# Performance work log

Hardware: AMD Instinct MI355X
Metric: run time of the kernel (lower is better)

## Reference

```python
import jax, jax.numpy as jnp
import numpy as np

T, B, F = 4096, 6, 128
H1, H3 = 512, 128  # 32*16 and 16*8


def run_lstm(x, Wi, Wh, b, h0, c0):
    """Standard LSTM over time-major x: [T, B, Fin] -> seq [T, B, H], (h, c)."""
    def step(carry, xt):
        h, c = carry
        z = xt @ Wi + h @ Wh + b           # [B, 4H]
        i, f, g, o = jnp.split(z, 4, axis=-1)
        c = jax.nn.sigmoid(f) * c + jax.nn.sigmoid(i) * jnp.tanh(g)
        h = jax.nn.sigmoid(o) * jnp.tanh(c)
        return (h, c), h
    (h, c), seq = jax.lax.scan(step, (h0, c0), x)
    return seq, h, c


def setup_inputs() -> dict:
    key = jax.random.key(0)
    ks = jax.random.split(key, 12)
    s = lambda fan_in: 1.0 / np.sqrt(fan_in)
    inp = {
        "x":   jax.random.normal(ks[0], (T, B, F), jnp.float32),
        "Wi1": jax.random.uniform(ks[1], (F, 4 * H1), jnp.float32, -s(H1), s(H1)),
        "Wh1": jax.random.uniform(ks[2], (H1, 4 * H1), jnp.float32, -s(H1), s(H1)),
        "b1":  jax.random.uniform(ks[3], (4 * H1,), jnp.float32, -s(H1), s(H1)),
        "Wi2": jax.random.uniform(ks[4], (H1, 4 * H1), jnp.float32, -s(H1), s(H1)),
        "Wh2": jax.random.uniform(ks[5], (H1, 4 * H1), jnp.float32, -s(H1), s(H1)),
        "b2":  jax.random.uniform(ks[6], (4 * H1,), jnp.float32, -s(H1), s(H1)),
        "Wi3": jax.random.uniform(ks[7], (H1, 4 * H3), jnp.float32, -s(H3), s(H3)),
        "Wh3": jax.random.uniform(ks[8], (H3, 4 * H3), jnp.float32, -s(H3), s(H3)),
        "b3":  jax.random.uniform(ks[9], (4 * H3,), jnp.float32, -s(H3), s(H3)),
        "Wl":  jax.random.uniform(ks[10], (H3, 1), jnp.float32, -s(H3), s(H3)),
        "bl":  jax.random.uniform(ks[11], (1,), jnp.float32, -s(H3), s(H3)),
    }
    return inp


def reference(x, Wi1, Wh1, b1, Wi2, Wh2, b2, Wi3, Wh3, b3, Wl, bl):
    z1 = jnp.zeros((B, H1), x.dtype)
    z3 = jnp.zeros((B, H3), x.dtype)
    seq, h, c = run_lstm(x, Wi1, Wh1, b1, z1, z1)
    seq, h, c = run_lstm(seq, Wi2, Wh2, b2, h, c)   # lstm2 reuses lstm1 final state
    seq, h, c = run_lstm(seq, Wi3, Wh3, b3, z3, z3) # lstm3 starts fresh
    return seq[-1] @ Wl + bl                         # [B, 1]
```

## Files before the change

kernel.cpp:

```cpp
#include <hip/hip_runtime.h>

#define TT 4096
#define NB 6

typedef unsigned int uint;
typedef unsigned long long u64;

__device__ __forceinline__ u64 ldp(const u64* p) {
  return __hip_atomic_load(p, __ATOMIC_RELAXED, __HIP_MEMORY_SCOPE_AGENT);
}
__device__ __forceinline__ void stp(u64* p, float v, uint s) {
  u64 x = ((u64)s << 32) | (u64)__float_as_uint(v);
  __hip_atomic_store(p, x, __ATOMIC_RELAXED, __HIP_MEMORY_SCOPE_AGENT);
}
__device__ __forceinline__ uint ldf(const uint* p) {
  return __hip_atomic_load(p, __ATOMIC_RELAXED, __HIP_MEMORY_SCOPE_AGENT);
}
__device__ __forceinline__ void stf(uint* p, uint v) {
  __hip_atomic_store(p, v, __ATOMIC_RELAXED, __HIP_MEMORY_SCOPE_AGENT);
}

__device__ __forceinline__ float sigm(float x) { return 1.f / (1.f + __expf(-x)); }
__device__ __forceinline__ float ftanh(float x) {
  x = fminf(fmaxf(x, -15.f), 15.f);
  const float e = __expf(-2.f * x);
  return (1.f - e) / (1.f + e);
}

__device__ __forceinline__ void lds_wave_fence() {
  asm volatile("s_waitcnt lgkmcnt(0)" ::: "memory");
  __builtin_amdgcn_sched_barrier(0);
}

__device__ __forceinline__ void poll6(const u64* rs, uint st, float out[6]) {
  u64 a0;
  for (;;) {
    a0 = ldp(rs);
    if ((uint)(a0 >> 32) == st) break;
    __builtin_amdgcn_s_sleep(1);
  }
  u64 a1, a2, a3, a4, a5;
  for (;;) {
    a1 = ldp(rs + 1); a2 = ldp(rs + 2); a3 = ldp(rs + 3);
    a4 = ldp(rs + 4); a5 = ldp(rs + 5);
    if (((uint)(a1 >> 32) == st) & ((uint)(a2 >> 32) == st) &
        ((uint)(a3 >> 32) == st) & ((uint)(a4 >> 32) == st) &
        ((uint)(a5 >> 32) == st)) break;
    __builtin_amdgcn_s_sleep(1);
  }
  out[0] = __uint_as_float((uint)a0); out[1] = __uint_as_float((uint)a1);
  out[2] = __uint_as_float((uint)a2); out[3] = __uint_as_float((uint)a3);
  out[4] = __uint_as_float((uint)a4); out[5] = __uint_as_float((uint)a5);
}

__device__ __forceinline__ void fma6(const float* vp, float w, float acc[6]) {
  const float2 v0 = *(const float2*)(vp);
  const float2 v1 = *(const float2*)(vp + 2);
  const float2 v2 = *(const float2*)(vp + 4);
  acc[0] += v0.x * w; acc[1] += v0.y * w; acc[2] += v1.x * w;
  acc[3] += v1.y * w; acc[4] += v2.x * w; acc[5] += v2.y * w;
}

__global__ __launch_bounds__(512, 2) void k_l1(
    const float* __restrict__ x, const float* __restrict__ Wi,
    const float* __restrict__ Wh, const float* __restrict__ bias,
    u64* h1ring, u64* h2ring, float* c1fin, float* seq1) {
  __shared__ float xl[2][128 * 6];
  __shared__ float hl[512 * 6];
  __shared__ float zred[16 * 32 * 8];
  __shared__ float zfin[32 * 6];
  __shared__ float bs[32];
  const int tid = threadIdx.x, wg = blockIdx.x;
  const int lane = tid & 63, w = tid >> 6;
  const int half = lane >> 5, c = lane & 31;
  const int u0 = wg * 8;
  const int gcol = ((c >> 3) * 512) + u0 + (c & 7);
  float wh[32], wx[8];
  {
    const int kh = w * 64 + half * 32, kx = w * 16 + half * 8;
#pragma unroll
    for (int kk = 0; kk < 32; ++kk) wh[kk] = Wh[(size_t)(kh + kk) * 2048 + gcol];
#pragma unroll
    for (int kk = 0; kk < 8; ++kk) wx[kk] = Wi[(size_t)(kx + kk) * 2048 + gcol];
  }
  if (tid < 32) bs[tid] = bias[((tid >> 3) * 512) + u0 + (tid & 7)];
  const int gj = tid / 6, gb = tid % 6;
  float creg = 0.f;
  {
    const float v0 = x[tid];
    float v1 = 0.f;
    if (tid < 256) v1 = x[512 + tid];
    xl[0][(tid & 127) * 6 + (tid >> 7)] = v0;
    if (tid < 256) { const int i = 512 + tid; xl[0][(i & 127) * 6 + (i >> 7)] = v1; }
  }
  __syncthreads();

  for (int t = 0; t < TT; ++t) {
    const float* xn = x + (size_t)((t + 1 < TT) ? t + 1 : TT - 1) * 768;
    const float v0p = xn[tid];
    float v1p = 0.f;
    if (tid < 256) v1p = xn[512 + tid];
    float acc[6] = {0, 0, 0, 0, 0, 0};
    {
      const float* xb = xl[t & 1] + (size_t)(w * 16 + half * 8) * 6;
#pragma unroll
      for (int kk = 0; kk < 8; ++kk) fma6(xb + kk * 6, wx[kk], acc);
    }
    {
      float hv[6];
      poll6(h1ring + (size_t)((t + 7) & 7) * 3072 + tid * 6, (uint)t, hv);
      float* hp = hl + tid * 6;
      *(float2*)(hp) = make_float2(hv[0], hv[1]);
      *(float2*)(hp + 2) = make_float2(hv[2], hv[3]);
      *(float2*)(hp + 4) = make_float2(hv[4], hv[5]);
    }
    lds_wave_fence();
    {
      const float* hb = hl + (size_t)(w * 64 + half * 32) * 6;
#pragma unroll
      for (int kk = 0; kk < 32; ++kk) fma6(hb + kk * 6, wh[kk], acc);
    }
    {
      float* zr = zred + (size_t)((w * 2 + half) * 32 + c) * 8;
      *(float4*)zr = make_float4(acc[0], acc[1], acc[2], acc[3]);
      *(float2*)(zr + 4) = make_float2(acc[4], acc[5]);
    }
    {
      float* xs = xl[(t + 1) & 1];
      xs[(tid & 127) * 6 + (tid >> 7)] = v0p;
      if (tid < 256) { const int i = 512 + tid; xs[(i & 127) * 6 + (i >> 7)] = v1p; }
    }
    __syncthreads();
    if (tid < 192) {
      const int cc = tid / 6, bb = tid % 6;
      float s = 0.f;
#pragma unroll
      for (int p = 0; p < 16; ++p) s += zred[(p * 32 + cc) * 8 + bb];
      zfin[cc * 6 + bb] = s;
    }
    __syncthreads();
    if (tid < 48) {
      __builtin_amdgcn_s_setprio(1);
      const float zi = zfin[(0 * 8 + gj) * 6 + gb] + bs[0 * 8 + gj];
      const float zf = zfin[(1 * 8 + gj) * 6 + gb] + bs[1 * 8 + gj];
      const float zg = zfin[(2 * 8 + gj) * 6 + gb] + bs[2 * 8 + gj];
      const float zo = zfin[(3 * 8 + gj) * 6 + gb] + bs[3 * 8 + gj];
      creg = sigm(zf) * creg + sigm(zi) * ftanh(zg);
      const float hval = sigm(zo) * ftanh(creg);
      const int gu = u0 + gj;
      stp(h1ring + (size_t)(t & 7) * 3072 + gu * 6 + gb, hval, (uint)(t + 1));
      seq1[(size_t)t * 4096 + gu * 8 + gb] = hval;
      if (t == TT - 1) {
        stp(h2ring + (size_t)7 * 3072 + gu * 6 + gb, hval, 0u);
        c1fin[gu * 6 + gb] = creg;
      }
      __builtin_amdgcn_s_setprio(0);
    }
  }
}

__global__ __launch_bounds__(512, 2) void k_l23(
    const float* __restrict__ seq1, const float* __restrict__ Wi2,
    const float* __restrict__ Wh2, const float* __restrict__ b2,
    const float* __restrict__ Wi3, const float* __restrict__ Wh3,
    const float* __restrict__ b3, const float* __restrict__ c1fin,
    u64* h2ring, u64* h3ring, float* h3fin, uint* flags3) {
  __shared__ float smem[13536];
  const int tid = threadIdx.x, wg = blockIdx.x;
  const int lane = tid & 63, w = tid >> 6;
  const int gj = tid / 6, gb = tid % 6;

  if (wg < 64) {
    float* xls = smem;
    float* hl = smem + 6144;
    float* zred = smem + 9216;
    float* zfin = smem + 13312;
    float* bsl = smem + 13504;
    const int half = lane >> 5, c = lane & 31;
    const int u0 = wg * 8;
    const int gcol = ((c >> 3) * 512) + u0 + (c & 7);
    float wh[32], wx[32];
    {
      const int kb = w * 64 + half * 32;
#pragma unroll
      for (int kk = 0; kk < 32; ++kk) {
        wh[kk] = Wh2[(size_t)(kb + kk) * 2048 + gcol];
        wx[kk] = Wi2[(size_t)(kb + kk) * 2048 + gcol];
      }
    }
    if (tid < 32) bsl[tid] = b2[((tid >> 3) * 512) + u0 + (tid & 7)];
    float creg = (tid < 48) ? c1fin[(u0 + gj) * 6 + gb] : 0.f;
    {
      const float4 s0 = *(const float4*)(seq1 + (size_t)tid * 8);
      const float4 s1 = *(const float4*)(seq1 + (size_t)tid * 8 + 4);
      float* xs = xls;
      *(float2*)(xs + tid * 6) = make_float2(s0.x, s0.y);
      *(float2*)(xs + tid * 6 + 2) = make_float2(s0.z, s0.w);
      *(float2*)(xs + tid * 6 + 4) = make_float2(s1.x, s1.y);
    }
    __syncthreads();

    for (int t = 0; t < TT; ++t) {
      if ((t & 3) == 0 && t >= 8 && tid < 48) {
        const uint need = (uint)(t - 4);
        while (ldf(flags3 + (tid & 7)) < need) __builtin_amdgcn_s_sleep(1);
      }
      const float* sn = seq1 + (size_t)((t + 1 < TT) ? t + 1 : TT - 1) * 4096;
      const float4 p0 = *(const float4*)(sn + (size_t)tid * 8);
      const float4 p1 = *(const float4*)(sn + (size_t)tid * 8 + 4);
      float acc[6] = {0, 0, 0, 0, 0, 0};
      {
        const float* xb = xls + (size_t)(t & 1) * 3072 + (size_t)(w * 64 + half * 32) * 6;
#pragma unroll
        for (int kk = 0; kk < 32; ++kk) fma6(xb + kk * 6, wx[kk], acc);
      }
      {
        float hv[6];
        poll6(h2ring + (size_t)((t + 7) & 7) * 3072 + tid * 6, (uint)t, hv);
        float* hp = hl + tid * 6;
        *(float2*)(hp) = make_float2(hv[0], hv[1]);
        *(float2*)(hp + 2) = make_float2(hv[2], hv[3]);
        *(float2*)(hp + 4) = make_float2(hv[4], hv[5]);
      }
      lds_wave_fence();
      {
        const float* hb = hl + (size_t)(w * 64 + half * 32) * 6;
#pragma unroll
        for (int kk = 0; kk < 32; ++kk) fma6(hb + kk * 6, wh[kk], acc);
      }
      {
        float* zr = zred + (size_t)((w * 2 + half) * 32 + c) * 8;
        *(float4*)zr = make_float4(acc[0], acc[1], acc[2], acc[3]);
        *(float2*)(zr + 4) = make_float2(acc[4], acc[5]);
      }
      {
        float* xs = xls + (size_t)((t + 1) & 1) * 3072;
        *(float2*)(xs + tid * 6) = make_float2(p0.x, p0.y);
        *(float2*)(xs + tid * 6 + 2) = make_float2(p0.z, p0.w);
        *(float2*)(xs + tid * 6 + 4) = make_float2(p1.x, p1.y);
      }
      __syncthreads();
      if (tid < 192) {
        const int cc = tid / 6, bb = tid % 6;
        float s = 0.f;
#pragma unroll
        for (int p = 0; p < 16; ++p) s += zred[(p * 32 + cc) * 8 + bb];
        zfin[cc * 6 + bb] = s;
      }
      __syncthreads();
      if (tid < 48) {
        __builtin_amdgcn_s_setprio(1);
        const float zi = zfin[(0 * 8 + gj) * 6 + gb] + bsl[0 * 8 + gj];
        const float zf = zfin[(1 * 8 + gj) * 6 + gb] + bsl[1 * 8 + gj];
        const float zg = zfin[(2 * 8 + gj) * 6 + gb] + bsl[2 * 8 + gj];
        const float zo = zfin[(3 * 8 + gj) * 6 + gb] + bsl[3 * 8 + gj];
        creg = sigm(zf) * creg + sigm(zi) * ftanh(zg);
        const float hval = sigm(zo) * ftanh(creg);
        stp(h2ring + (size_t)(t & 7) * 3072 + (u0 + gj) * 6 + gb, hval, (uint)(t + 1));
        __builtin_amdgcn_s_setprio(0);
      }
    }
  } else {
    float* hl2 = smem;
    float* hl3 = smem + 3072;
    float* zred = smem + 3840;
    float* zfin = smem + 7936;
    float* bsl = smem + 8320;
    const int wg3 = wg - 64;
    const int c = lane;
    const int u0 = wg3 * 16;
    const int gcol = ((c >> 4) * 128) + u0 + (c & 15);
    float wxh2[64], wh3[16];
#pragma unroll
    for (int kk = 0; kk < 64; ++kk) wxh2[kk] = Wi3[(size_t)(w * 64 + kk) * 512 + gcol];
#pragma unroll
    for (int kk = 0; kk < 16; ++kk) wh3[kk] = Wh3[(size_t)(w * 16 + kk) * 512 + gcol];
    if (tid < 64) bsl[tid] = b3[((tid >> 4) * 128) + u0 + (tid & 15)];
    float creg = 0.f;

    for (int t = 0; t < TT; ++t) {
      {
        const u64* rs3 = h3ring + (size_t)((t + 7) & 7) * 768;
        const int a = 96 * w + lane;
        u64 v;
        for (;;) { v = ldp(rs3 + a); if ((uint)(v >> 32) == (uint)t) break; __builtin_amdgcn_s_sleep(1); }
        hl3[a] = __uint_as_float((uint)v);
        if (lane < 32) {
          const int a2 = a + 64;
          u64 v2;
          for (;;) { v2 = ldp(rs3 + a2); if ((uint)(v2 >> 32) == (uint)t) break; __builtin_amdgcn_s_sleep(1); }
          hl3[a2] = __uint_as_float((uint)v2);
        }
      }
      {
        float hv[6];
        poll6(h2ring + (size_t)(t & 7) * 3072 + tid * 6, (uint)(t + 1), hv);
        float* hp = hl2 + tid * 6;
        *(float2*)(hp) = make_float2(hv[0], hv[1]);
        *(float2*)(hp + 2) = make_float2(hv[2], hv[3]);
        *(float2*)(hp + 4) = make_float2(hv[4], hv[5]);
      }
      lds_wave_fence();
      float acc[6] = {0, 0, 0, 0, 0, 0};
      {
        const float* hb = hl2 + (size_t)(w * 64) * 6;
#pragma unroll
        for (int kk = 0; kk < 64; ++kk) fma6(hb + kk * 6, wxh2[kk], acc);
        const float* h3b = hl3 + (size_t)(w * 16) * 6;
#pragma unroll
        for (int kk = 0; kk < 16; ++kk) fma6(h3b + kk * 6, wh3[kk], acc);
      }
      {
        float* zr = zred + (size_t)(w * 64 + c) * 8;
        *(float4*)zr = make_float4(acc[0], acc[1], acc[2], acc[3]);
        *(float2*)(zr + 4) = make_float2(acc[4], acc[5]);
      }
      __syncthreads();
      if (tid == 0) stf(flags3 + wg3, (uint)(t + 1));
      if (tid < 384) {
        const int cc = tid / 6, bb = tid % 6;
        float s = 0.f;
#pragma unroll
        for (int p = 0; p < 8; ++p) s += zred[(p * 64 + cc) * 8 + bb];
        zfin[cc * 6 + bb] = s;
      }
      __syncthreads();
      if (tid < 96) {
        __builtin_amdgcn_s_setprio(1);
        const float zi = zfin[(0 * 16 + gj) * 6 + gb] + bsl[0 * 16 + gj];
        const float zf = zfin[(1 * 16 + gj) * 6 + gb] + bsl[1 * 16 + gj];
        const float zg = zfin[(2 * 16 + gj) * 6 + gb] + bsl[2 * 16 + gj];
        const float zo = zfin[(3 * 16 + gj) * 6 + gb] + bsl[3 * 16 + gj];
        creg = sigm(zf) * creg + sigm(zi) * ftanh(zg);
        const float hval = sigm(zo) * ftanh(creg);
        stp(h3ring + (size_t)(t & 7) * 768 + (u0 + gj) * 6 + gb, hval, (uint)(t + 1));
        if (t == TT - 1) h3fin[(u0 + gj) * 6 + gb] = hval;
        __builtin_amdgcn_s_setprio(0);
      }
    }
  }
}

__global__ void k_out(const float* __restrict__ h3fin, const float* __restrict__ Wl,
                      const float* __restrict__ bl, float* __restrict__ out) {
  const int tid = threadIdx.x;
  float p[NB] = {0, 0, 0, 0, 0, 0};
  for (int k = tid; k < 128; k += 64) {
    const float w = Wl[k];
#pragma unroll
    for (int b = 0; b < NB; ++b) p[b] += h3fin[k * 6 + b] * w;
  }
#pragma unroll
  for (int off = 32; off > 0; off >>= 1) {
#pragma unroll
    for (int b = 0; b < NB; ++b) p[b] += __shfl_down(p[b], off);
  }
  if (tid == 0) {
#pragma unroll
    for (int b = 0; b < NB; ++b) out[b] = p[b] + bl[0];
  }
}

extern "C" void kernel_launch(void* const* d_in, const int* in_sizes, int n_in,
                              void* d_out, int out_size, void* d_ws, size_t ws_size,
                              hipStream_t stream) {
  (void)in_sizes; (void)n_in; (void)out_size;
  const float* x   = (const float*)d_in[0];
  const float* Wi1 = (const float*)d_in[1];
  const float* Wh1 = (const float*)d_in[2];
  const float* b1  = (const float*)d_in[3];
  const float* Wi2 = (const float*)d_in[4];
  const float* Wh2 = (const float*)d_in[5];
  const float* b2  = (const float*)d_in[6];
  const float* Wi3 = (const float*)d_in[7];
  const float* Wh3 = (const float*)d_in[8];
  const float* b3  = (const float*)d_in[9];
  const float* Wl  = (const float*)d_in[10];
  const float* bl  = (const float*)d_in[11];

  char* wsb = (char*)d_ws;
  u64*  h1ring = (u64*)(wsb + 0);
  u64*  h2ring = (u64*)(wsb + 196608);
  u64*  h3ring = (u64*)(wsb + 393216);
  float* c1fin = (float*)(wsb + 442368);
  float* h3fin = (float*)(wsb + 454656);
  uint* flags3 = (uint*)(wsb + 457728);
  float* seq1  = (float*)(wsb + 458752);

  const size_t need = 458752 + (size_t)TT * 512 * 8 * sizeof(float);
  if (ws_size < need) {
    hipMemsetAsync(d_out, 0, 6 * sizeof(float), stream);
    return;
  }

  hipMemsetAsync(d_ws, 0, 458752, stream);

  k_l1<<<64, 512, 0, stream>>>(x, Wi1, Wh1, b1, h1ring, h2ring, c1fin, seq1);
  k_l23<<<72, 512, 0, stream>>>(seq1, Wi2, Wh2, b2, Wi3, Wh3, b3, c1fin,
                                h2ring, h3ring, h3fin, flags3);
  k_out<<<1, 64, 0, stream>>>(h3fin, Wl, bl, (float*)d_out);
}
```

Before: 44.91 ms.

## Halve workgroup count with 16 units per block and fuse gate reduction

Layer-1 and layer-2 blocks now each own 16 hidden units instead of 8. Each thread holds 64 recurrent weights in registers, and each wave covers a full K slice, so fewer blocks take part in the cross-block h-ring exchange. The separate zfin reduction pass and one barrier are folded into the gate threads, which sum the 8 wave partials directly from a padded zred buffer. Polling now reads all six slots together and spins up to 64 times before sleeping. In exchange, register pressure rises (launch bounds lose the 2-blocks hint), each block does twice the FMA work per step, and a trailing barrier is added in the layer-3 path.

```diff
diff --git a/kernel.cpp b/kernel.cpp
--- a/kernel.cpp
+++ b/kernel.cpp
@@ -33,24 +33,31 @@
 }
 
 __device__ __forceinline__ void poll6(const u64* rs, uint st, float out[6]) {
-  u64 a0;
+  int spins = 0;
   for (;;) {
-    a0 = ldp(rs);
-    if ((uint)(a0 >> 32) == st) break;
-    __builtin_amdgcn_s_sleep(1);
-  }
-  u64 a1, a2, a3, a4, a5;
+    const u64 a0 = ldp(rs + 0), a1 = ldp(rs + 1), a2 = ldp(rs + 2);
+    const u64 a3 = ldp(rs + 3), a4 = ldp(rs + 4), a5 = ldp(rs + 5);
+    if (((uint)(a0 >> 32) == st) & ((uint)(a1 >> 32) == st) &
+        ((uint)(a2 >> 32) == st) & ((uint)(a3 >> 32) == st) &
+        ((uint)(a4 >> 32) == st) & ((uint)(a5 >> 32) == st)) {
+      out[0] = __uint_as_float((uint)a0); out[1] = __uint_as_float((uint)a1);
+      out[2] = __uint_as_float((uint)a2); out[3] = __uint_as_float((uint)a3);
+      out[4] = __uint_as_float((uint)a4); out[5] = __uint_as_float((uint)a5);
+      return;
+    }
+    if (++spins >= 64) { __builtin_amdgcn_s_sleep(1); spins = 0; }
+  }
+}
+__device__ __forceinline__ void poll2(const u64* rs, uint st, float out[2]) {
+  int spins = 0;
   for (;;) {
-    a1 = ldp(rs + 1); a2 = ldp(rs + 2); a3 = ldp(rs + 3);
-    a4 = ldp(rs + 4); a5 = ldp(rs + 5);
-    if (((uint)(a1 >> 32) == st) & ((uint)(a2 >> 32) == st) &
-        ((uint)(a3 >> 32) == st) & ((uint)(a4 >> 32) == st) &
-        ((uint)(a5 >> 32) == st)) break;
-    __builtin_amdgcn_s_sleep(1);
-  }
-  out[0] = __uint_as_float((uint)a0); out[1] = __uint_as_float((uint)a1);
-  out[2] = __uint_as_float((uint)a2); out[3] = __uint_as_float((uint)a3);
-  out[4] = __uint_as_float((uint)a4); out[5] = __uint_as_float((uint)a5);
+    const u64 a0 = ldp(rs + 0), a1 = ldp(rs + 1);
+    if (((uint)(a0 >> 32) == st) & ((uint)(a1 >> 32) == st)) {
+      out[0] = __uint_as_float((uint)a0); out[1] = __uint_as_float((uint)a1);
+      return;
+    }
+    if (++spins >= 64) { __builtin_amdgcn_s_sleep(1); spins = 0; }
+  }
 }
 
 __device__ __forceinline__ void fma6(const float* vp, float w, float acc[6]) {
@@ -61,29 +68,26 @@
   acc[3] += v1.y * w; acc[4] += v2.x * w; acc[5] += v2.y * w;
 }
 
-__global__ __launch_bounds__(512, 2) void k_l1(
+#define ZSTRIDE 520
+
+__global__ __launch_bounds__(512) void k_l1(
     const float* __restrict__ x, const float* __restrict__ Wi,
     const float* __restrict__ Wh, const float* __restrict__ bias,
     u64* h1ring, u64* h2ring, float* c1fin, float* seq1) {
   __shared__ float xl[2][128 * 6];
   __shared__ float hl[512 * 6];
-  __shared__ float zred[16 * 32 * 8];
-  __shared__ float zfin[32 * 6];
-  __shared__ float bs[32];
+  __shared__ float zred[8 * ZSTRIDE];
+  __shared__ float bs[64];
   const int tid = threadIdx.x, wg = blockIdx.x;
-  const int lane = tid & 63, w = tid >> 6;
-  const int half = lane >> 5, c = lane & 31;
-  const int u0 = wg * 8;
-  const int gcol = ((c >> 3) * 512) + u0 + (c & 7);
-  float wh[32], wx[8];
-  {
-    const int kh = w * 64 + half * 32, kx = w * 16 + half * 8;
-#pragma unroll
-    for (int kk = 0; kk < 32; ++kk) wh[kk] = Wh[(size_t)(kh + kk) * 2048 + gcol];
-#pragma unroll
-    for (int kk = 0; kk < 8; ++kk) wx[kk] = Wi[(size_t)(kx + kk) * 2048 + gcol];
-  }
-  if (tid < 32) bs[tid] = bias[((tid >> 3) * 512) + u0 + (tid & 7)];
+  const int c = tid & 63, w = tid >> 6;
+  const int u0 = wg * 16;
+  const int gcol = ((c >> 4) * 512) + u0 + (c & 15);
+  float wh[64], wx[16];
+#pragma unroll
+  for (int kk = 0; kk < 64; ++kk) wh[kk] = Wh[(size_t)(w * 64 + kk) * 2048 + gcol];
+#pragma unroll
+  for (int kk = 0; kk < 16; ++kk) wx[kk] = Wi[(size_t)(w * 16 + kk) * 2048 + gcol];
+  if (tid < 64) bs[tid] = bias[((tid >> 4) * 512) + u0 + (tid & 15)];
   const int gj = tid / 6, gb = tid % 6;
   float creg = 0.f;
   {
@@ -102,9 +106,9 @@
     if (tid < 256) v1p = xn[512 + tid];
     float acc[6] = {0, 0, 0, 0, 0, 0};
     {
-      const float* xb = xl[t & 1] + (size_t)(w * 16 + half * 8) * 6;
-#pragma unroll
-      for (int kk = 0; kk < 8; ++kk) fma6(xb + kk * 6, wx[kk], acc);
+      const float* xb = xl[t & 1] + (size_t)(w * 16) * 6;
+#pragma unroll
+      for (int kk = 0; kk < 16; ++kk) fma6(xb + kk * 6, wx[kk], acc);
     }
     {
       float hv[6];
@@ -116,12 +120,12 @@
     }
     lds_wave_fence();
     {
-      const float* hb = hl + (size_t)(w * 64 + half * 32) * 6;
-#pragma unroll
-      for (int kk = 0; kk < 32; ++kk) fma6(hb + kk * 6, wh[kk], acc);
-    }
-    {
-      float* zr = zred + (size_t)((w * 2 + half) * 32 + c) * 8;
+      const float* hb = hl + (size_t)(w * 64) * 6;
+#pragma unroll
+      for (int kk = 0; kk < 64; ++kk) fma6(hb + kk * 6, wh[kk], acc);
+    }
+    {
+      float* zr = zred + w * ZSTRIDE + c * 8;
       *(float4*)zr = make_float4(acc[0], acc[1], acc[2], acc[3]);
       *(float2*)(zr + 4) = make_float2(acc[4], acc[5]);
     }
@@ -131,22 +135,19 @@
       if (tid < 256) { const int i = 512 + tid; xs[(i & 127) * 6 + (i >> 7)] = v1p; }
     }
     __syncthreads();
-    if (tid < 192) {
-      const int cc = tid / 6, bb = tid % 6;
-      float s = 0.f;
-#pragma unroll
-      for (int p = 0; p < 16; ++p) s += zred[(p * 32 + cc) * 8 + bb];
-      zfin[cc * 6 + bb] = s;
-    }
-    __syncthreads();
-    if (tid < 48) {
+    if (tid < 96) {
       __builtin_amdgcn_s_setprio(1);
-      const float zi = zfin[(0 * 8 + gj) * 6 + gb] + bs[0 * 8 + gj];
-      const float zf = zfin[(1 * 8 + gj) * 6 + gb] + bs[1 * 8 + gj];
-      const float zg = zfin[(2 * 8 + gj) * 6 + gb] + bs[2 * 8 + gj];
-      const float zo = zfin[(3 * 8 + gj) * 6 + gb] + bs[3 * 8 + gj];
-      creg = sigm(zf) * creg + sigm(zi) * ftanh(zg);
-      const float hval = sigm(zo) * ftanh(creg);
+      float z[4];
+#pragma unroll
+      for (int g = 0; g < 4; ++g) {
+        const int cc = g * 16 + gj;
+        float s = 0.f;
+#pragma unroll
+        for (int p = 0; p < 8; ++p) s += zred[p * ZSTRIDE + cc * 8 + gb];
+        z[g] = s + bs[cc];
+      }
+      creg = sigm(z[1]) * creg + sigm(z[0]) * ftanh(z[2]);
+      const float hval = sigm(z[3]) * ftanh(creg);
       const int gu = u0 + gj;
       stp(h1ring + (size_t)(t & 7) * 3072 + gu * 6 + gb, hval, (uint)(t + 1));
       seq1[(size_t)t * 4096 + gu * 8 + gb] = hval;
@@ -159,60 +160,55 @@
   }
 }
 
-__global__ __launch_bounds__(512, 2) void k_l23(
+__global__ __launch_bounds__(512) void k_l23(
     const float* __restrict__ seq1, const float* __restrict__ Wi2,
     const float* __restrict__ Wh2, const float* __restrict__ b2,
     const float* __restrict__ Wi3, const float* __restrict__ Wh3,
     const float* __restrict__ b3, const float* __restrict__ c1fin,
     u64* h2ring, u64* h3ring, float* h3fin, uint* flags3) {
-  __shared__ float smem[13536];
+  __shared__ float smem[13440];
   const int tid = threadIdx.x, wg = blockIdx.x;
-  const int lane = tid & 63, w = tid >> 6;
+  const int c = tid & 63, w = tid >> 6;
   const int gj = tid / 6, gb = tid % 6;
 
-  if (wg < 64) {
+  if (wg < 32) {
     float* xls = smem;
     float* hl = smem + 6144;
     float* zred = smem + 9216;
-    float* zfin = smem + 13312;
-    float* bsl = smem + 13504;
-    const int half = lane >> 5, c = lane & 31;
-    const int u0 = wg * 8;
-    const int gcol = ((c >> 3) * 512) + u0 + (c & 7);
-    float wh[32], wx[32];
-    {
-      const int kb = w * 64 + half * 32;
-#pragma unroll
-      for (int kk = 0; kk < 32; ++kk) {
-        wh[kk] = Wh2[(size_t)(kb + kk) * 2048 + gcol];
-        wx[kk] = Wi2[(size_t)(kb + kk) * 2048 + gcol];
-      }
-    }
-    if (tid < 32) bsl[tid] = b2[((tid >> 3) * 512) + u0 + (tid & 7)];
-    float creg = (tid < 48) ? c1fin[(u0 + gj) * 6 + gb] : 0.f;
+    float* bsl = smem + 13376;
+    const int u0 = wg * 16;
+    const int gcol = ((c >> 4) * 512) + u0 + (c & 15);
+    float wh[64], wx[64];
+#pragma unroll
+    for (int kk = 0; kk < 64; ++kk) {
+      wh[kk] = Wh2[(size_t)(w * 64 + kk) * 2048 + gcol];
+      wx[kk] = Wi2[(size_t)(w * 64 + kk) * 2048 + gcol];
+    }
+    if (tid < 64) bsl[tid] = b2[((tid >> 4) * 512) + u0 + (tid & 15)];
+    float creg = (tid < 96) ? c1fin[(u0 + gj) * 6 + gb] : 0.f;
     {
       const float4 s0 = *(const float4*)(seq1 + (size_t)tid * 8);
-      const float4 s1 = *(const float4*)(seq1 + (size_t)tid * 8 + 4);
-      float* xs = xls;
-      *(float2*)(xs + tid * 6) = make_float2(s0.x, s0.y);
-      *(float2*)(xs + tid * 6 + 2) = make_float2(s0.z, s0.w);
-      *(float2*)(xs + tid * 6 + 4) = make_float2(s1.x, s1.y);
+      const float2 s1 = *(const float2*)(seq1 + (size_t)tid * 8 + 4);
+      float* xs = xls + tid * 6;
+      *(float2*)(xs) = make_float2(s0.x, s0.y);
+      *(float2*)(xs + 2) = make_float2(s0.z, s0.w);
+      *(float2*)(xs + 4) = make_float2(s1.x, s1.y);
     }
     __syncthreads();
 
     for (int t = 0; t < TT; ++t) {
-      if ((t & 3) == 0 && t >= 8 && tid < 48) {
+      if ((t & 3) == 0 && t >= 8 && tid < 8) {
         const uint need = (uint)(t - 4);
-        while (ldf(flags3 + (tid & 7)) < need) __builtin_amdgcn_s_sleep(1);
+        while (ldf(flags3 + tid) < need) __builtin_amdgcn_s_sleep(1);
       }
       const float* sn = seq1 + (size_t)((t + 1 < TT) ? t + 1 : TT - 1) * 4096;
       const float4 p0 = *(const float4*)(sn + (size_t)tid * 8);
-      const float4 p1 = *(const float4*)(sn + (size_t)tid * 8 + 4);
+      const float2 p1 = *(const float2*)(sn + (size_t)tid * 8 + 4);
       float acc[6] = {0, 0, 0, 0, 0, 0};
       {
-        const float* xb = xls + (size_t)(t & 1) * 3072 + (size_t)(w * 64 + half * 32) * 6;
-#pragma unroll
-        for (int kk = 0; kk < 32; ++kk) fma6(xb + kk * 6, wx[kk], acc);
+        const float* xb = xls + (size_t)(t & 1) * 3072 + (size_t)(w * 64) * 6;
+#pragma unroll
+        for (int kk = 0; kk < 64; ++kk) fma6(xb + kk * 6, wx[kk], acc);
       }
       {
         float hv[6];
@@ -224,51 +220,45 @@
       }
       lds_wave_fence();
       {
-        const float* hb = hl + (size_t)(w * 64 + half * 32) * 6;
-#pragma unroll
-        for (int kk = 0; kk < 32; ++kk) fma6(hb + kk * 6, wh[kk], acc);
-      }
-      {
-        float* zr = zred + (size_t)((w * 2 + half) * 32 + c) * 8;
+        const float* hb = hl + (size_t)(w * 64) * 6;
+#pragma unroll
+        for (int kk = 0; kk < 64; ++kk) fma6(hb + kk * 6, wh[kk], acc);
+      }
+      {
+        float* zr = zred + w * ZSTRIDE + c * 8;
         *(float4*)zr = make_float4(acc[0], acc[1], acc[2], acc[3]);
         *(float2*)(zr + 4) = make_float2(acc[4], acc[5]);
       }
       {
-        float* xs = xls + (size_t)((t + 1) & 1) * 3072;
-        *(float2*)(xs + tid * 6) = make_float2(p0.x, p0.y);
-        *(float2*)(xs + tid * 6 + 2) = make_float2(p0.z, p0.w);
-        *(float2*)(xs + tid * 6 + 4) = make_float2(p1.x, p1.y);
+        float* xs = xls + (size_t)((t + 1) & 1) * 3072 + tid * 6;
+        *(float2*)(xs) = make_float2(p0.x, p0.y);
+        *(float2*)(xs + 2) = make_float2(p0.z, p0.w);
+        *(float2*)(xs + 4) = make_float2(p1.x, p1.y);
       }
       __syncthreads();
-      if (tid < 192) {
-        const int cc = tid / 6, bb = tid % 6;
-        float s = 0.f;
-#pragma unroll
-        for (int p = 0; p < 16; ++p) s += zred[(p * 32 + cc) * 8 + bb];
-        zfin[cc * 6 + bb] = s;
-      }
-      __syncthreads();
-      if (tid < 48) {
+      if (tid < 96) {
         __builtin_amdgcn_s_setprio(1);
-        const float zi = zfin[(0 * 8 + gj) * 6 + gb] + bsl[0 * 8 + gj];
-        const float zf = zfin[(1 * 8 + gj) * 6 + gb] + bsl[1 * 8 + gj];
-        const float zg = zfin[(2 * 8 + gj) * 6 + gb] + bsl[2 * 8 + gj];
-        const float zo = zfin[(3 * 8 + gj) * 6 + gb] + bsl[3 * 8 + gj];
-        creg = sigm(zf) * creg + sigm(zi) * ftanh(zg);
-        const float hval = sigm(zo) * ftanh(creg);
+        float z[4];
+#pragma unroll
+        for (int g = 0; g < 4; ++g) {
+          const int cc = g * 16 + gj;
+          float s = 0.f;
+#pragma unroll
+          for (int p = 0; p < 8; ++p) s += zred[p * ZSTRIDE + cc * 8 + gb];
+          z[g] = s + bsl[cc];
+        }
+        creg = sigm(z[1]) * creg + sigm(z[0]) * ftanh(z[2]);
+        const float hval = sigm(z[3]) * ftanh(creg);
         stp(h2ring + (size_t)(t & 7) * 3072 + (u0 + gj) * 6 + gb, hval, (uint)(t + 1));
         __builtin_amdgcn_s_setprio(0);
       }
     }
   } else {
-    float* hl2 = smem;
+    float* hl = smem;
     float* hl3 = smem + 3072;
     float* zred = smem + 3840;
-    float* zfin = smem + 7936;
-    float* bsl = smem + 8320;
-    const int wg3 = wg - 64;
-    const int c = lane;
-    const int u0 = wg3 * 16;
+    float* bsl = smem + 8000;
+    const int wg3 = wg - 32, u0 = wg3 * 16;
     const int gcol = ((c >> 4) * 128) + u0 + (c & 15);
     float wxh2[64], wh3[16];
 #pragma unroll
@@ -279,23 +269,17 @@
     float creg = 0.f;
 
     for (int t = 0; t < TT; ++t) {
-      {
-        const u64* rs3 = h3ring + (size_t)((t + 7) & 7) * 768;
-        const int a = 96 * w + lane;
-        u64 v;
-        for (;;) { v = ldp(rs3 + a); if ((uint)(v >> 32) == (uint)t) break; __builtin_amdgcn_s_sleep(1); }
-        hl3[a] = __uint_as_float((uint)v);
-        if (lane < 32) {
-          const int a2 = a + 64;
-          u64 v2;
-          for (;;) { v2 = ldp(rs3 + a2); if ((uint)(v2 >> 32) == (uint)t) break; __builtin_amdgcn_s_sleep(1); }
-          hl3[a2] = __uint_as_float((uint)v2);
-        }
+      const int lane = tid & 63;
+      if (lane < 48) {
+        float h2v[2];
+        poll2(h3ring + (size_t)((t + 7) & 7) * 768 + 96 * w + 2 * lane, (uint)t, h2v);
+        hl3[96 * w + 2 * lane] = h2v[0];
+        hl3[96 * w + 2 * lane + 1] = h2v[1];
       }
       {
         float hv[6];
         poll6(h2ring + (size_t)(t & 7) * 3072 + tid * 6, (uint)(t + 1), hv);
-        float* hp = hl2 + tid * 6;
+        float* hp = hl + tid * 6;
         *(float2*)(hp) = make_float2(hv[0], hv[1]);
         *(float2*)(hp + 2) = make_float2(hv[2], hv[3]);
         *(float2*)(hp + 4) = make_float2(hv[4], hv[5]);
@@ -303,40 +287,38 @@
       lds_wave_fence();
       float acc[6] = {0, 0, 0, 0, 0, 0};
       {
-        const float* hb = hl2 + (size_t)(w * 64) * 6;
+        const float* hb = hl + (size_t)(w * 64) * 6;
 #pragma unroll
         for (int kk = 0; kk < 64; ++kk) fma6(hb + kk * 6, wxh2[kk], acc);
-        const float* h3b = hl3 + (size_t)(w * 16) * 6;
+        const float* h3b = hl3 + 96 * w;
 #pragma unroll
         for (int kk = 0; kk < 16; ++kk) fma6(h3b + kk * 6, wh3[kk], acc);
       }
       {
-        float* zr = zred + (size_t)(w * 64 + c) * 8;
+        float* zr = zred + w * ZSTRIDE + c * 8;
         *(float4*)zr = make_float4(acc[0], acc[1], acc[2], acc[3]);
         *(float2*)(zr + 4) = make_float2(acc[4], acc[5]);
       }
       __syncthreads();
       if (tid == 0) stf(flags3 + wg3, (uint)(t + 1));
-      if (tid < 384) {
-        const int cc = tid / 6, bb = tid % 6;
-        float s = 0.f;
-#pragma unroll
-        for (int p = 0; p < 8; ++p) s += zred[(p * 64 + cc) * 8 + bb];
-        zfin[cc * 6 + bb] = s;
-      }
-      __syncthreads();
       if (tid < 96) {
         __builtin_amdgcn_s_setprio(1);
-        const float zi = zfin[(0 * 16 + gj) * 6 + gb] + bsl[0 * 16 + gj];
-        const float zf = zfin[(1 * 16 + gj) * 6 + gb] + bsl[1 * 16 + gj];
-        const float zg = zfin[(2 * 16 + gj) * 6 + gb] + bsl[2 * 16 + gj];
-        const float zo = zfin[(3 * 16 + gj) * 6 + gb] + bsl[3 * 16 + gj];
-        creg = sigm(zf) * creg + sigm(zi) * ftanh(zg);
-        const float hval = sigm(zo) * ftanh(creg);
+        float z[4];
+#pragma unroll
+        for (int g = 0; g < 4; ++g) {
+          const int cc = g * 16 + gj;
+          float s = 0.f;
+#pragma unroll
+          for (int p = 0; p < 8; ++p) s += zred[p * ZSTRIDE + cc * 8 + gb];
+          z[g] = s + bsl[cc];
+        }
+        creg = sigm(z[1]) * creg + sigm(z[0]) * ftanh(z[2]);
+        const float hval = sigm(z[3]) * ftanh(creg);
         stp(h3ring + (size_t)(t & 7) * 768 + (u0 + gj) * 6 + gb, hval, (uint)(t + 1));
         if (t == TT - 1) h3fin[(u0 + gj) * 6 + gb] = hval;
         __builtin_amdgcn_s_setprio(0);
       }
+      __syncthreads();
     }
   }
 }
@@ -395,8 +377,8 @@
 
   hipMemsetAsync(d_ws, 0, 458752, stream);
 
-  k_l1<<<64, 512, 0, stream>>>(x, Wi1, Wh1, b1, h1ring, h2ring, c1fin, seq1);
-  k_l23<<<72, 512, 0, stream>>>(seq1, Wi2, Wh2, b2, Wi3, Wh3, b3, c1fin,
+  k_l1<<<32, 512, 0, stream>>>(x, Wi1, Wh1, b1, h1ring, h2ring, c1fin, seq1);
+  k_l23<<<40, 512, 0, stream>>>(seq1, Wi2, Wh2, b2, Wi3, Wh3, b3, c1fin,
                                 h2ring, h3ring, h3fin, flags3);
   k_out<<<1, 64, 0, stream>>>(h3fin, Wl, bl, (float*)d_out);
 }
```

Result: slower. 163.9 ms (+265.0%).
